# Optimization experiments

Hardware: AMD Instinct MI355X
Metric: run time of the kernel (lower is better)

## Reference

```python
import jax, jax.numpy as jnp
import numpy as np

N_NODES = 100000
N_EDGES = 1600000
IN_DIM, HID, OUT_DIM = 128, 64, 1


def _sage_conv(x, src, dst, wl, wr, b, num_nodes):
    # PyG SAGEConv (aggr='mean', root_weight=True):
    #   out = lin_l(mean_{j in N(i)} x_j) + lin_r(x_i), bias lives in lin_l
    msgs = x[src]                                                  # [E, d] gather
    agg = jax.ops.segment_sum(msgs, dst, num_segments=num_nodes)  # [N, d]
    deg = jax.ops.segment_sum(jnp.ones((src.shape[0],), x.dtype), dst,
                              num_segments=num_nodes)              # [N]
    agg = agg / jnp.maximum(deg, 1.0)[:, None]                     # mean aggregation
    return agg @ wl + x @ wr + b


def setup_inputs() -> dict:
    key = jax.random.key(0)
    ks = jax.random.split(key, 12)
    x = jax.random.normal(ks[0], (N_NODES, IN_DIM), dtype=jnp.float32)
    edge_index = jax.random.randint(ks[1], (2, N_EDGES), 0, N_NODES, dtype=jnp.int64)

    def glorot(k, fan_in, fan_out):
        s = jnp.sqrt(2.0 / (fan_in + fan_out)).astype(jnp.float32)
        return jax.random.normal(k, (fan_in, fan_out), dtype=jnp.float32) * s

    return {
        "x": x,
        "edge_index": edge_index,
        "wl0": glorot(ks[2], IN_DIM, HID), "wr0": glorot(ks[3], IN_DIM, HID),
        "b0": jnp.zeros((HID,), jnp.float32),
        "wl1": glorot(ks[4], HID, HID), "wr1": glorot(ks[5], HID, HID),
        "b1": jnp.zeros((HID,), jnp.float32),
        "wl2": glorot(ks[6], HID, OUT_DIM), "wr2": glorot(ks[7], HID, OUT_DIM),
        "b2": jnp.zeros((OUT_DIM,), jnp.float32),
    }


def reference(x, edge_index, wl0, wr0, b0, wl1, wr1, b1, wl2, wr2, b2):
    src, dst = edge_index[0], edge_index[1]
    n = x.shape[0]
    # layer 0: conv -> relu (dropout is identity in eval mode)
    h = jax.nn.relu(_sage_conv(x, src, dst, wl0, wr0, b0, n))
    # layer 1
    h = jax.nn.relu(_sage_conv(h, src, dst, wl1, wr1, b1, n))
    # final layer + sigmoid
    h = _sage_conv(h, src, dst, wl2, wr2, b2, n)
    return jax.nn.sigmoid(h)
```

## Files before the change

kernel.cpp:

```cpp
#include <hip/hip_runtime.h>
#include <hip/hip_bf16.h>
#include <math.h>


#define SHIFT 7
#define BKT 128
#define CHUNK 4096
#define CAP 4096
#define LCAP 2560
#define HSTR 72

typedef __bf16 bf16_t;
typedef bf16_t bf16x8 __attribute__((ext_vector_type(8)));
typedef float f32x4 __attribute__((ext_vector_type(4)));

#define B16LO(u) __uint_as_float((u) << 16)
#define B16HI(u) __uint_as_float((u) & 0xffff0000u)

#define ADD8(P, V) { P##0 += B16LO(V.x); P##1 += B16HI(V.x); \
                     P##2 += B16LO(V.y); P##3 += B16HI(V.y); \
                     P##4 += B16LO(V.z); P##5 += B16HI(V.z); \
                     P##6 += B16LO(V.w); P##7 += B16HI(V.w); }
#define BFLY(P, M) { P##0 += __shfl_xor(P##0, M); P##1 += __shfl_xor(P##1, M); \
                     P##2 += __shfl_xor(P##2, M); P##3 += __shfl_xor(P##3, M); \
                     P##4 += __shfl_xor(P##4, M); P##5 += __shfl_xor(P##5, M); \
                     P##6 += __shfl_xor(P##6, M); P##7 += __shfl_xor(P##7, M); }

__global__ __launch_bounds__(256) void init_k(const float* __restrict__ wl0,
                                              const float* __restrict__ wr0,
                                              const float* __restrict__ wl1,
                                              const float* __restrict__ wr1,
                                              bf16_t* __restrict__ w0t,
                                              bf16_t* __restrict__ w1t,
                                              int* __restrict__ bcnt,
                                              int NB, int nbP) {
    if ((int)blockIdx.x >= nbP) {
        for (int i = threadIdx.x; i < NB; i += 256) bcnt[i] = 0;
        return;
    }
    int idx = blockIdx.x * 256 + threadIdx.x;
    if (idx < 128 * 128) {
        int j = idx >> 7, k = idx & 127;
        float v = (j < 64) ? wl0[k * 64 + j] : wr0[k * 64 + (j - 64)];
        w0t[idx] = (bf16_t)v;
    } else if (idx < 128 * 128 + 128 * 64) {
        int i2 = idx - 128 * 128;
        int j = i2 >> 6, k = i2 & 63;
        float v = (j < 64) ? wl1[k * 64 + j] : wr1[k * 64 + (j - 64)];
        w1t[i2] = (bf16_t)v;
    }
}

__global__ __launch_bounds__(256) void scatter_gemm0(const int* __restrict__ srcv,
                                                     const int* __restrict__ dstv,
                                                     int* __restrict__ bcnt,
                                                     int* __restrict__ bucketed,
                                                     int E, int NB, int nbC,
                                                     const float* __restrict__ x,
                                                     const bf16_t* __restrict__ w0t,
                                                     bf16_t* __restrict__ y, int N) {
    if ((int)blockIdx.x >= nbC) {
        const int bid = blockIdx.x - nbC;
        const int t = threadIdx.x;
        const int lane = t & 63;
        const int wv = t >> 6;
        const int r0 = bid * 64 + wv * 16;
        const int rr = lane & 15;
        const int quad = lane >> 4;
        const int row_store = r0 + rr;
        int row = (row_store < N) ? row_store : (N - 1);

        bf16x8 xf[4];
#pragma unroll
        for (int kk = 0; kk < 4; ++kk) {
            const float* ap = &x[(size_t)row * 128 + kk * 32 + quad * 8];
            float4 f0 = *(const float4*)ap;
            float4 f1 = *(const float4*)(ap + 4);
            union { bf16x8 v; bf16_t h[8]; } u;
            u.h[0] = (bf16_t)f0.x; u.h[1] = (bf16_t)f0.y;
            u.h[2] = (bf16_t)f0.z; u.h[3] = (bf16_t)f0.w;
            u.h[4] = (bf16_t)f1.x; u.h[5] = (bf16_t)f1.y;
            u.h[6] = (bf16_t)f1.z; u.h[7] = (bf16_t)f1.w;
            xf[kk] = u.v;
        }
#pragma unroll
        for (int c = 0; c < 8; ++c) {
            f32x4 acc = {0.f, 0.f, 0.f, 0.f};
#pragma unroll
            for (int kk = 0; kk < 4; ++kk) {
                bf16x8 wf = *(const bf16x8*)&w0t[(size_t)(c * 16 + rr) * 128 + kk * 32 + quad * 8];
                acc = __builtin_amdgcn_mfma_f32_16x16x32_bf16(wf, xf[kk], acc, 0, 0, 0);
            }
            if (row_store < N) {
                union { bf16_t h[4]; uint2 u; } p;
                p.h[0] = (bf16_t)acc[0]; p.h[1] = (bf16_t)acc[1];
                p.h[2] = (bf16_t)acc[2]; p.h[3] = (bf16_t)acc[3];
                *(uint2*)&y[(size_t)row_store * 128 + c * 16 + quad * 4] = p.u;
            }
        }
        return;
    }

    __shared__ int hist[1024];
    __shared__ int offl[1024];
    __shared__ int basel[1024];
    __shared__ int partial[256];
    __shared__ int posA[CHUNK];
    __shared__ int valA[CHUNK];
    const int t = threadIdx.x;
    for (int i = t; i < NB; i += 256) hist[i] = 0;
    __syncthreads();

    const int cbase = blockIdx.x * CHUNK;
    int bk[CHUNK / 256], rk[CHUNK / 256], vv[CHUNK / 256];
#pragma unroll
    for (int k = 0; k < CHUNK / 256; ++k) {
        int e = cbase + t + k * 256;
        if (e < E) {
            int d = dstv[e];
            int s = srcv[e];
            int b = d >> SHIFT;
            bk[k] = b;
            rk[k] = atomicAdd(&hist[b], 1);
            vv[k] = (s << SHIFT) | (d & (BKT - 1));
        } else {
            bk[k] = -1;
        }
    }
    __syncthreads();

    for (int b = t; b < NB; b += 256) {
        int c = hist[b];
        basel[b] = c ? (b * CAP + atomicAdd(&bcnt[b], c)) : 0;
    }
    {
        int g = t * 4;
        int a0 = (g + 0 < NB) ? hist[g + 0] : 0;
        int a1 = (g + 1 < NB) ? hist[g + 1] : 0;
        int a2 = (g + 2 < NB) ? hist[g + 2] : 0;
        int a3 = (g + 3 < NB) ? hist[g + 3] : 0;
        int sum = a0 + a1 + a2 + a3;
        partial[t] = sum;
        __syncthreads();
        for (int d = 1; d < 256; d <<= 1) {
            int xsc = (t >= d) ? partial[t - d] : 0;
            __syncthreads();
            partial[t] += xsc;
            __syncthreads();
        }
        int ex = partial[t] - sum;
        if (g + 0 < NB) offl[g + 0] = ex;
        if (g + 1 < NB) offl[g + 1] = ex + a0;
        if (g + 2 < NB) offl[g + 2] = ex + a0 + a1;
        if (g + 3 < NB) offl[g + 3] = ex + a0 + a1 + a2;
    }
    __syncthreads();

    int nloc = E - cbase;
    if (nloc > CHUNK) nloc = CHUNK;
#pragma unroll
    for (int k = 0; k < CHUNK / 256; ++k) {
        if (bk[k] >= 0) {
            int slot = offl[bk[k]] + rk[k];
            posA[slot] = basel[bk[k]] + rk[k];
            valA[slot] = vv[k];
        }
    }
    __syncthreads();
    for (int j = t; j < nloc; j += 256) bucketed[posA[j]] = valA[j];
}

__global__ __launch_bounds__(256) void sort_agg0_gemm1(const int* __restrict__ bucketed,
                                                       const int* __restrict__ bcnt,
                                                       int2* __restrict__ od,
                                                       int* __restrict__ csr,
                                                       const bf16_t* __restrict__ y,
                                                       const float* __restrict__ bias,
                                                       const bf16_t* __restrict__ w1t,
                                                       bf16_t* __restrict__ y2,
                                                       int N, int NB) {
    __shared__ int cnt[BKT];
    __shared__ int sc[BKT];
    __shared__ int cur[BKT];
    __shared__ int lcsr[LCAP];
    __shared__ bf16_t hlds[BKT * HSTR];
    const int t = threadIdx.x;
    const int b = blockIdx.x;
    const int ebase = b * CAP;
    const int ecnt = bcnt[b];
    const int eend = ebase + ecnt;

    if (t < BKT) cnt[t] = 0;
    __syncthreads();
    int wreg[CAP / 256];
#pragma unroll
    for (int k = 0; k < CAP / 256; ++k) {
        int i = ebase + t + k * 256;
        if (i < eend) {
            wreg[k] = bucketed[i];
            atomicAdd(&cnt[wreg[k] & (BKT - 1)], 1);
        }
    }
    __syncthreads();
    int v = (t < BKT) ? cnt[t] : 0;
    if (t < BKT) sc[t] = v;
    __syncthreads();
    for (int d = 1; d < BKT; d <<= 1) {
        int xsc = (t < BKT && t >= d) ? sc[t - d] : 0;
        __syncthreads();
        if (t < BKT) sc[t] += xsc;
        __syncthreads();
    }
    if (t < BKT) {
        int ex = sc[t] - v;
        cur[t] = ex;
        int dst = (b << SHIFT) + t;
        if (dst < N) od[dst] = make_int2(ebase + ex, v);
    }
    __syncthreads();
#pragma unroll
    for (int k = 0; k < CAP / 256; ++k) {
        int i = ebase + t + k * 256;
        if (i < eend) {
            int w = wreg[k];
            int p = atomicAdd(&cur[w & (BKT - 1)], 1);
            int s = w >> SHIFT;
            csr[ebase + p] = s;
            if (p < LCAP) lcsr[p] = s;
        }
    }
    __syncthreads();

    const int lane = t & 63;
    const int wv = t >> 6;
    const int oct = lane >> 3;
    const int ch = (lane & 7) * 8;
    const int gbase = b << SHIFT;
    const float4 bv0 = *(const float4*)&bias[ch];
    const float4 bv1 = *(const float4*)&bias[ch + 4];

    for (int k = 0; k < 32; ++k) {
        const int n = wv * 32 + k;
        const int gi = gbase + n;
        const int d = (gi < N) ? cnt[n] : 0;
        const int bas = sc[n] - cnt[n];
        int sidx = 0;
        if (lane < d) {
            int slot = bas + lane;
            sidx = (slot < LCAP) ? lcsr[slot] : csr[ebase + slot];
        }
        float a0 = 0.f, a1 = 0.f, a2 = 0.f, a3 = 0.f;
        float a4 = 0.f, a5 = 0.f, a6 = 0.f, a7 = 0.f;
        const int nblk = d >> 3;
        const int pm = (nblk < 8) ? nblk : 8;
        int p = 0;
        for (; p + 2 <= pm; p += 2) {
            int s0 = __shfl(sidx, 8 * p + oct);
            int s1 = __shfl(sidx, 8 * p + 8 + oct);
            uint4 v0 = *(const uint4*)&y[(size_t)s0 * 128 + ch];
            uint4 v1 = *(const uint4*)&y[(size_t)s1 * 128 + ch];
            ADD8(a, v0); ADD8(a, v1);
        }
        for (; p < pm; ++p) {
            int s0 = __shfl(sidx, 8 * p + oct);
            uint4 v0 = *(const uint4*)&y[(size_t)s0 * 128 + ch];
            ADD8(a, v0);
        }
        for (; p < nblk; ++p) {
            int s0 = csr[ebase + bas + 8 * p + oct];
            uint4 v0 = *(const uint4*)&y[(size_t)s0 * 128 + ch];
            ADD8(a, v0);
        }
        {
            int te = 8 * nblk + oct;
            int tec = (te < 64) ? te : 63;
            int s_t = __shfl(sidx, tec);
            if (te < d) {
                int s0 = (te < 64) ? s_t : csr[ebase + bas + te];
                uint4 v0 = *(const uint4*)&y[(size_t)s0 * 128 + ch];
                ADD8(a, v0);
            }
        }

        BFLY(a, 8); BFLY(a, 16); BFLY(a, 32);

        if (gi < N) {
            float inv = 1.f / ((d > 0) ? (float)d : 1.f);
            uint4 vs = *(const uint4*)&y[(size_t)gi * 128 + 64 + ch];
            float v0 = fmaxf(a0 * inv + B16LO(vs.x) + bv0.x, 0.f);
            float v1 = fmaxf(a1 * inv + B16HI(vs.x) + bv0.y, 0.f);
            float v2 = fmaxf(a2 * inv + B16LO(vs.y) + bv0.z, 0.f);
            float v3 = fmaxf(a3 * inv + B16HI(vs.y) + bv0.w, 0.f);
            float v4 = fmaxf(a4 * inv + B16LO(vs.z) + bv1.x, 0.f);
            float v5 = fmaxf(a5 * inv + B16HI(vs.z) + bv1.y, 0.f);
            float v6 = fmaxf(a6 * inv + B16LO(vs.w) + bv1.z, 0.f);
            float v7 = fmaxf(a7 * inv + B16HI(vs.w) + bv1.w, 0.f);
            if (oct == 0) {
                union { bf16_t bb[8]; uint4 u; } pk;
                pk.bb[0] = (bf16_t)v0; pk.bb[1] = (bf16_t)v1;
                pk.bb[2] = (bf16_t)v2; pk.bb[3] = (bf16_t)v3;
                pk.bb[4] = (bf16_t)v4; pk.bb[5] = (bf16_t)v5;
                pk.bb[6] = (bf16_t)v6; pk.bb[7] = (bf16_t)v7;
                *(uint4*)&hlds[n * HSTR + ch] = pk.u;
            }
        }
    }
    __syncthreads();

    const int rr = lane & 15;
    const int quad = lane >> 4;
#pragma unroll
    for (int half = 0; half < 2; ++half) {
        const int rloc = wv * 32 + half * 16 + rr;
        const int row_store = gbase + rloc;
        bf16x8 xf[2];
#pragma unroll
        for (int kk = 0; kk < 2; ++kk)
            xf[kk] = *(const bf16x8*)&hlds[rloc * HSTR + kk * 32 + quad * 8];
#pragma unroll
        for (int c = 0; c < 8; ++c) {
            f32x4 acc = {0.f, 0.f, 0.f, 0.f};
#pragma unroll
            for (int kk = 0; kk < 2; ++kk) {
                bf16x8 wf = *(const bf16x8*)&w1t[(size_t)(c * 16 + rr) * 64 + kk * 32 + quad * 8];
                acc = __builtin_amdgcn_mfma_f32_16x16x32_bf16(wf, xf[kk], acc, 0, 0, 0);
            }
            if (row_store < N) {
                union { bf16_t h[4]; uint2 u; } p;
                p.h[0] = (bf16_t)acc[0]; p.h[1] = (bf16_t)acc[1];
                p.h[2] = (bf16_t)acc[2]; p.h[3] = (bf16_t)acc[3];
                *(uint2*)&y2[(size_t)row_store * 128 + c * 16 + quad * 4] = p.u;
            }
        }
    }
}

__global__ __launch_bounds__(256) void agg1(const bf16_t* __restrict__ y,
                                            const int* __restrict__ csr,
                                            const int2* __restrict__ od,
                                            const float* __restrict__ bias,
                                            const float* __restrict__ wl2,
                                            const float* __restrict__ wr2,
                                            float* __restrict__ sl,
                                            float* __restrict__ sr, int N) {
    const int lane = threadIdx.x & 63;
    const int oct = lane >> 3;
    const int ch = (lane & 7) * 8;
    const int nw = gridDim.x * 4;

    int i = blockIdx.x * 4 + (threadIdx.x >> 6);
    int2 odc = (i < N) ? od[i] : make_int2(0, 0);
    int sidx = 0;
    if (i < N) sidx = (lane < odc.y) ? csr[odc.x + lane] : 0;

    while (i < N) {
        const int inext = i + nw;
        int2 odn = (inext < N) ? od[inext] : make_int2(0, 0);

        const int base = odc.x;
        const int d = odc.y;
        float a0 = 0.f, a1 = 0.f, a2 = 0.f, a3 = 0.f;
        float a4 = 0.f, a5 = 0.f, a6 = 0.f, a7 = 0.f;
        const int nblk = d >> 3;
        const int pm = (nblk < 8) ? nblk : 8;
        int p = 0;
        for (; p + 2 <= pm; p += 2) {
            int s0 = __shfl(sidx, 8 * p + oct);
            int s1 = __shfl(sidx, 8 * p + 8 + oct);
            uint4 v0 = *(const uint4*)&y[(size_t)s0 * 128 + ch];
            uint4 v1 = *(const uint4*)&y[(size_t)s1 * 128 + ch];
            ADD8(a, v0); ADD8(a, v1);
        }
        for (; p < pm; ++p) {
            int s0 = __shfl(sidx, 8 * p + oct);
            uint4 v0 = *(const uint4*)&y[(size_t)s0 * 128 + ch];
            ADD8(a, v0);
        }
        for (; p < nblk; ++p) {
            int s0 = csr[base + 8 * p + oct];
            uint4 v0 = *(const uint4*)&y[(size_t)s0 * 128 + ch];
            ADD8(a, v0);
        }
        {
            int te = 8 * nblk + oct;
            int tec = (te < 64) ? te : 63;
            int s_t = __shfl(sidx, tec);
            if (te < d) {
                int s0 = (te < 64) ? s_t : csr[base + te];
                uint4 v0 = *(const uint4*)&y[(size_t)s0 * 128 + ch];
                ADD8(a, v0);
            }
        }

        int sidxn = 0;
        if (inext < N) sidxn = (lane < odn.y) ? csr[odn.x + lane] : 0;

        BFLY(a, 8); BFLY(a, 16); BFLY(a, 32);

        float inv = 1.f / ((d > 0) ? (float)d : 1.f);
        uint4 vs = *(const uint4*)&y[(size_t)i * 128 + 64 + ch];
        float4 bv0 = *(const float4*)&bias[ch];
        float4 bv1 = *(const float4*)&bias[ch + 4];
        float v0 = fmaxf(a0 * inv + B16LO(vs.x) + bv0.x, 0.f);
        float v1 = fmaxf(a1 * inv + B16HI(vs.x) + bv0.y, 0.f);
        float v2 = fmaxf(a2 * inv + B16LO(vs.y) + bv0.z, 0.f);
        float v3 = fmaxf(a3 * inv + B16HI(vs.y) + bv0.w, 0.f);
        float v4 = fmaxf(a4 * inv + B16LO(vs.z) + bv1.x, 0.f);
        float v5 = fmaxf(a5 * inv + B16HI(vs.z) + bv1.y, 0.f);
        float v6 = fmaxf(a6 * inv + B16LO(vs.w) + bv1.z, 0.f);
        float v7 = fmaxf(a7 * inv + B16HI(vs.w) + bv1.w, 0.f);

        {
            float4 w0 = *(const float4*)&wl2[ch];
            float4 w1 = *(const float4*)&wl2[ch + 4];
            float4 u0 = *(const float4*)&wr2[ch];
            float4 u1 = *(const float4*)&wr2[ch + 4];
            float a = v0 * w0.x + v1 * w0.y + v2 * w0.z + v3 * w0.w +
                      v4 * w1.x + v5 * w1.y + v6 * w1.z + v7 * w1.w;
            float b = v0 * u0.x + v1 * u0.y + v2 * u0.z + v3 * u0.w +
                      v4 * u1.x + v5 * u1.y + v6 * u1.z + v7 * u1.w;
            a += __shfl_xor(a, 1); b += __shfl_xor(b, 1);
            a += __shfl_xor(a, 2); b += __shfl_xor(b, 2);
            a += __shfl_xor(a, 4); b += __shfl_xor(b, 4);
            if (lane == 0) { sl[i] = a; sr[i] = b; }
        }

        odc = odn;
        sidx = sidxn;
        i = inext;
    }
}

__global__ __launch_bounds__(256) void final_k(const float* __restrict__ sl,
                                               const float* __restrict__ sr,
                                               const int* __restrict__ csr,
                                               const int2* __restrict__ od,
                                               const float* __restrict__ b2,
                                               float* __restrict__ out, int N) {
    int wid = blockIdx.x * 4 + (threadIdx.x >> 6);
    if (wid >= N) return;
    const int lane = threadIdx.x & 63;
    const int2 odv = od[wid];
    const int base = odv.x;
    const int d = odv.y;
    float acc = 0.f;
    for (int e = lane; e < d; e += 64) acc += sl[csr[base + e]];
#pragma unroll
    for (int off = 32; off; off >>= 1) acc += __shfl_xor(acc, off);
    if (lane == 0) {
        float m = (d > 0) ? (float)d : 1.f;
        float v = acc / m + sr[wid] + b2[0];
        out[wid] = 1.f / (1.f + expf(-v));
    }
}

extern "C" void kernel_launch(void* const* d_in, const int* in_sizes, int n_in,
                              void* d_out, int out_size, void* d_ws, size_t ws_size,
                              hipStream_t stream) {
    const float* x  = (const float*)d_in[0];
    const int*  ei  = (const int*)d_in[1];
    const float* wl0 = (const float*)d_in[2];
    const float* wr0 = (const float*)d_in[3];
    const float* b0  = (const float*)d_in[4];
    const float* wl1 = (const float*)d_in[5];
    const float* wr1 = (const float*)d_in[6];
    const float* b1  = (const float*)d_in[7];
    const float* wl2 = (const float*)d_in[8];
    const float* wr2 = (const float*)d_in[9];
    const float* b2  = (const float*)d_in[10];
    float* out = (float*)d_out;

    const int E = in_sizes[1] / 2;
    const int N = out_size;
    const int* srcv = ei;
    const int* dstv = ei + E;
    const int NB = (N + BKT - 1) >> SHIFT;

    char* ws = (char*)d_ws;
    size_t o = 0;
    auto take = [&](size_t nbytes) -> void* {
        void* p = ws + o;
        o = (o + nbytes + 255) & ~(size_t)255;
        return p;
    };
    int2* od      = (int2*)take((size_t)N * 8);
    int* bcnt     = (int*)take((size_t)(NB + 2) * 4);
    int* bucketed = (int*)take((size_t)NB * CAP * 4);
    int* csr      = (int*)take((size_t)NB * CAP * 4);
    bf16_t* w0t   = (bf16_t*)take(128 * 128 * 2);
    bf16_t* w1t   = (bf16_t*)take(128 * 64 * 2);
    bf16_t* y     = (bf16_t*)take((size_t)N * 128 * 2);
    bf16_t* y2    = (bf16_t*)take((size_t)N * 128 * 2);
    float* sl     = (float*)take((size_t)N * 4);
    float* sr     = (float*)take((size_t)N * 4);
    (void)ws_size;

    const int nbC = (E + CHUNK - 1) / CHUNK;
    const int nbP = (128 * 128 + 128 * 64 + 255) / 256;
    const int nbW = (N + 3) / 4;
    const int nbG = (N + 63) / 64;
    const int nbA = 2048;

    init_k<<<nbP + 1, 256, 0, stream>>>(wl0, wr0, wl1, wr1, w0t, w1t, bcnt, NB, nbP);
    scatter_gemm0<<<nbC + nbG, 256, 0, stream>>>(srcv, dstv, bcnt, bucketed, E, NB, nbC,
                                                 x, w0t, y, N);

    sort_agg0_gemm1<<<NB, 256, 0, stream>>>(bucketed, bcnt, od, csr, y, b0, w1t,
                                            y2, N, NB);
    agg1<<<nbA, 256, 0, stream>>>(y2, csr, od, b1, wl2, wr2, sl, sr, N);
    final_k<<<nbW, 256, 0, stream>>>(sl, sr, csr, od, b2, out, N);
}
```

Baseline: 289.7 us.

## Fuse all stages into one persistent cooperative kernel with grid syncs

Replaces the five separate kernel launches with a single persistent cooperative kernel that loops over virtual blocks and uses grid-wide syncs between the weight prep, bucketing/GEMM0, sort/aggregate, and final stages. It also splits the left and right projection outputs into separate 64-wide buffers so the neighbour gather reads a compact array, and halves the edge chunk size so the shared-memory footprint permits higher occupancy. The aim is to remove launch gaps and tail effects between stages. In exchange, grid syncs serialize all blocks at each stage boundary, and the fixed persistent grid may balance work worse than a full launch.

```diff
diff --git a/kernel.cpp b/kernel.cpp
--- a/kernel.cpp
+++ b/kernel.cpp
@@ -1,14 +1,16 @@
 #include <hip/hip_runtime.h>
+#include <hip/hip_cooperative_groups.h>
 #include <hip/hip_bf16.h>
 #include <math.h>
 
 
 #define SHIFT 7
 #define BKT 128
-#define CHUNK 4096
+#define CHUNK 2048
 #define CAP 4096
 #define LCAP 2560
 #define HSTR 72
+#define SMEM_BYTES 30208
 
 typedef __bf16 bf16_t;
 typedef bf16_t bf16x8 __attribute__((ext_vector_type(8)));
@@ -26,267 +28,365 @@
                      P##4 += __shfl_xor(P##4, M); P##5 += __shfl_xor(P##5, M); \
                      P##6 += __shfl_xor(P##6, M); P##7 += __shfl_xor(P##7, M); }
 
-__global__ __launch_bounds__(256) void init_k(const float* __restrict__ wl0,
-                                              const float* __restrict__ wr0,
-                                              const float* __restrict__ wl1,
-                                              const float* __restrict__ wr1,
-                                              bf16_t* __restrict__ w0t,
-                                              bf16_t* __restrict__ w1t,
-                                              int* __restrict__ bcnt,
-                                              int NB, int nbP) {
-    if ((int)blockIdx.x >= nbP) {
-        for (int i = threadIdx.x; i < NB; i += 256) bcnt[i] = 0;
-        return;
-    }
-    int idx = blockIdx.x * 256 + threadIdx.x;
-    if (idx < 128 * 128) {
-        int j = idx >> 7, k = idx & 127;
-        float v = (j < 64) ? wl0[k * 64 + j] : wr0[k * 64 + (j - 64)];
-        w0t[idx] = (bf16_t)v;
-    } else if (idx < 128 * 128 + 128 * 64) {
-        int i2 = idx - 128 * 128;
-        int j = i2 >> 6, k = i2 & 63;
-        float v = (j < 64) ? wl1[k * 64 + j] : wr1[k * 64 + (j - 64)];
-        w1t[i2] = (bf16_t)v;
-    }
-}
-
-__global__ __launch_bounds__(256) void scatter_gemm0(const int* __restrict__ srcv,
-                                                     const int* __restrict__ dstv,
-                                                     int* __restrict__ bcnt,
-                                                     int* __restrict__ bucketed,
-                                                     int E, int NB, int nbC,
-                                                     const float* __restrict__ x,
-                                                     const bf16_t* __restrict__ w0t,
-                                                     bf16_t* __restrict__ y, int N) {
-    if ((int)blockIdx.x >= nbC) {
-        const int bid = blockIdx.x - nbC;
-        const int t = threadIdx.x;
-        const int lane = t & 63;
-        const int wv = t >> 6;
-        const int r0 = bid * 64 + wv * 16;
-        const int rr = lane & 15;
-        const int quad = lane >> 4;
-        const int row_store = r0 + rr;
-        int row = (row_store < N) ? row_store : (N - 1);
-
-        bf16x8 xf[4];
-#pragma unroll
-        for (int kk = 0; kk < 4; ++kk) {
-            const float* ap = &x[(size_t)row * 128 + kk * 32 + quad * 8];
-            float4 f0 = *(const float4*)ap;
-            float4 f1 = *(const float4*)(ap + 4);
-            union { bf16x8 v; bf16_t h[8]; } u;
-            u.h[0] = (bf16_t)f0.x; u.h[1] = (bf16_t)f0.y;
-            u.h[2] = (bf16_t)f0.z; u.h[3] = (bf16_t)f0.w;
-            u.h[4] = (bf16_t)f1.x; u.h[5] = (bf16_t)f1.y;
-            u.h[6] = (bf16_t)f1.z; u.h[7] = (bf16_t)f1.w;
-            xf[kk] = u.v;
-        }
-#pragma unroll
-        for (int c = 0; c < 8; ++c) {
-            f32x4 acc = {0.f, 0.f, 0.f, 0.f};
-#pragma unroll
-            for (int kk = 0; kk < 4; ++kk) {
-                bf16x8 wf = *(const bf16x8*)&w0t[(size_t)(c * 16 + rr) * 128 + kk * 32 + quad * 8];
-                acc = __builtin_amdgcn_mfma_f32_16x16x32_bf16(wf, xf[kk], acc, 0, 0, 0);
-            }
-            if (row_store < N) {
-                union { bf16_t h[4]; uint2 u; } p;
-                p.h[0] = (bf16_t)acc[0]; p.h[1] = (bf16_t)acc[1];
-                p.h[2] = (bf16_t)acc[2]; p.h[3] = (bf16_t)acc[3];
-                *(uint2*)&y[(size_t)row_store * 128 + c * 16 + quad * 4] = p.u;
-            }
-        }
-        return;
-    }
-
-    __shared__ int hist[1024];
-    __shared__ int offl[1024];
-    __shared__ int basel[1024];
-    __shared__ int partial[256];
-    __shared__ int posA[CHUNK];
-    __shared__ int valA[CHUNK];
+struct KParams {
+    const int* srcv; const int* dstv;
+    int* bcnt; int* bucketed; int* csr; int2* od;
+    const float* x;
+    bf16_t* w0t; bf16_t* w1t;
+    bf16_t* yl; bf16_t* yr; bf16_t* y2l; bf16_t* y2r;
+    float* sl; float* sr;
+    const float* wl0; const float* wr0; const float* wl1; const float* wr1;
+    const float* b0; const float* b1;
+    const float* wl2; const float* wr2; const float* b2;
+    float* out;
+    int N, E, NB, nvC, nvG;
+};
+
+__global__ __launch_bounds__(256, 5) void fused_all(KParams p) {
+    namespace cg = cooperative_groups;
+    cg::grid_group grid = cg::this_grid();
+    __shared__ __align__(16) char smem[SMEM_BYTES];
     const int t = threadIdx.x;
-    for (int i = t; i < NB; i += 256) hist[i] = 0;
-    __syncthreads();
-
-    const int cbase = blockIdx.x * CHUNK;
-    int bk[CHUNK / 256], rk[CHUNK / 256], vv[CHUNK / 256];
-#pragma unroll
-    for (int k = 0; k < CHUNK / 256; ++k) {
-        int e = cbase + t + k * 256;
-        if (e < E) {
-            int d = dstv[e];
-            int s = srcv[e];
-            int b = d >> SHIFT;
-            bk[k] = b;
-            rk[k] = atomicAdd(&hist[b], 1);
-            vv[k] = (s << SHIFT) | (d & (BKT - 1));
+    const int nbg = gridDim.x;
+    const int lane = t & 63;
+    const int wv = t >> 6;
+
+    for (int idx = blockIdx.x * 256 + t; idx < 128 * 128 + 128 * 64;
+         idx += nbg * 256) {
+        if (idx < 128 * 128) {
+            int j = idx >> 7, k = idx & 127;
+            float v = (j < 64) ? p.wl0[k * 64 + j] : p.wr0[k * 64 + (j - 64)];
+            p.w0t[idx] = (bf16_t)v;
         } else {
-            bk[k] = -1;
+            int i2 = idx - 128 * 128;
+            int j = i2 >> 6, k = i2 & 63;
+            float v = (j < 64) ? p.wl1[k * 64 + j] : p.wr1[k * 64 + (j - 64)];
+            p.w1t[i2] = (bf16_t)v;
         }
     }
-    __syncthreads();
-
-    for (int b = t; b < NB; b += 256) {
-        int c = hist[b];
-        basel[b] = c ? (b * CAP + atomicAdd(&bcnt[b], c)) : 0;
-    }
+    for (int i = blockIdx.x * 256 + t; i < p.NB; i += nbg * 256) p.bcnt[i] = 0;
+    grid.sync();
+
     {
-        int g = t * 4;
-        int a0 = (g + 0 < NB) ? hist[g + 0] : 0;
-        int a1 = (g + 1 < NB) ? hist[g + 1] : 0;
-        int a2 = (g + 2 < NB) ? hist[g + 2] : 0;
-        int a3 = (g + 3 < NB) ? hist[g + 3] : 0;
-        int sum = a0 + a1 + a2 + a3;
-        partial[t] = sum;
-        __syncthreads();
-        for (int d = 1; d < 256; d <<= 1) {
-            int xsc = (t >= d) ? partial[t - d] : 0;
-            __syncthreads();
-            partial[t] += xsc;
-            __syncthreads();
-        }
-        int ex = partial[t] - sum;
-        if (g + 0 < NB) offl[g + 0] = ex;
-        if (g + 1 < NB) offl[g + 1] = ex + a0;
-        if (g + 2 < NB) offl[g + 2] = ex + a0 + a1;
-        if (g + 3 < NB) offl[g + 3] = ex + a0 + a1 + a2;
-    }
-    __syncthreads();
-
-    int nloc = E - cbase;
-    if (nloc > CHUNK) nloc = CHUNK;
-#pragma unroll
-    for (int k = 0; k < CHUNK / 256; ++k) {
-        if (bk[k] >= 0) {
-            int slot = offl[bk[k]] + rk[k];
-            posA[slot] = basel[bk[k]] + rk[k];
-            valA[slot] = vv[k];
+        int* hist = (int*)smem;
+        int* offl = hist + 1024;
+        int* basel = offl + 1024;
+        int* partial = basel + 1024;
+        int* posA = partial + 256;
+        int* valA = posA + CHUNK;
+        const int nvTot = p.nvC + p.nvG;
+        for (int vb = blockIdx.x; vb < nvTot; vb += nbg) {
+            if (vb >= p.nvC) {
+                const int bid = vb - p.nvC;
+                const int r0 = bid * 64 + wv * 16;
+                const int rr = lane & 15;
+                const int quad = lane >> 4;
+                const int row_store = r0 + rr;
+                int row = (row_store < p.N) ? row_store : (p.N - 1);
+                bf16x8 xf[4];
+#pragma unroll
+                for (int kk = 0; kk < 4; ++kk) {
+                    const float* ap = &p.x[(size_t)row * 128 + kk * 32 + quad * 8];
+                    float4 f0 = *(const float4*)ap;
+                    float4 f1 = *(const float4*)(ap + 4);
+                    union { bf16x8 v; bf16_t h[8]; } u;
+                    u.h[0] = (bf16_t)f0.x; u.h[1] = (bf16_t)f0.y;
+                    u.h[2] = (bf16_t)f0.z; u.h[3] = (bf16_t)f0.w;
+                    u.h[4] = (bf16_t)f1.x; u.h[5] = (bf16_t)f1.y;
+                    u.h[6] = (bf16_t)f1.z; u.h[7] = (bf16_t)f1.w;
+                    xf[kk] = u.v;
+                }
+#pragma unroll
+                for (int c = 0; c < 8; ++c) {
+                    f32x4 acc = {0.f, 0.f, 0.f, 0.f};
+#pragma unroll
+                    for (int kk = 0; kk < 4; ++kk) {
+                        bf16x8 wf = *(const bf16x8*)&p.w0t[(size_t)(c * 16 + rr) * 128 + kk * 32 + quad * 8];
+                        acc = __builtin_amdgcn_mfma_f32_16x16x32_bf16(wf, xf[kk], acc, 0, 0, 0);
+                    }
+                    if (row_store < p.N) {
+                        union { bf16_t h[4]; uint2 u; } pk;
+                        pk.h[0] = (bf16_t)acc[0]; pk.h[1] = (bf16_t)acc[1];
+                        pk.h[2] = (bf16_t)acc[2]; pk.h[3] = (bf16_t)acc[3];
+                        if (c < 4)
+                            *(uint2*)&p.yl[(size_t)row_store * 64 + c * 16 + quad * 4] = pk.u;
+                        else
+                            *(uint2*)&p.yr[(size_t)row_store * 64 + (c - 4) * 16 + quad * 4] = pk.u;
+                    }
+                }
+                continue;
+            }
+            for (int i = t; i < p.NB; i += 256) hist[i] = 0;
+            __syncthreads();
+            const int cbase = vb * CHUNK;
+            int bk[CHUNK / 256], rk[CHUNK / 256], vvv[CHUNK / 256];
+#pragma unroll
+            for (int k = 0; k < CHUNK / 256; ++k) {
+                int e = cbase + t + k * 256;
+                if (e < p.E) {
+                    int d = p.dstv[e];
+                    int s = p.srcv[e];
+                    int b = d >> SHIFT;
+                    bk[k] = b;
+                    rk[k] = atomicAdd(&hist[b], 1);
+                    vvv[k] = (s << SHIFT) | (d & (BKT - 1));
+                } else {
+                    bk[k] = -1;
+                }
+            }
+            __syncthreads();
+            for (int b = t; b < p.NB; b += 256) {
+                int c = hist[b];
+                basel[b] = c ? (b * CAP + atomicAdd(&p.bcnt[b], c)) : 0;
+            }
+            {
+                int g = t * 4;
+                int a0 = (g + 0 < p.NB) ? hist[g + 0] : 0;
+                int a1 = (g + 1 < p.NB) ? hist[g + 1] : 0;
+                int a2 = (g + 2 < p.NB) ? hist[g + 2] : 0;
+                int a3 = (g + 3 < p.NB) ? hist[g + 3] : 0;
+                int sum = a0 + a1 + a2 + a3;
+                partial[t] = sum;
+                __syncthreads();
+                for (int d = 1; d < 256; d <<= 1) {
+                    int xsc = (t >= d) ? partial[t - d] : 0;
+                    __syncthreads();
+                    partial[t] += xsc;
+                    __syncthreads();
+                }
+                int ex = partial[t] - sum;
+                if (g + 0 < p.NB) offl[g + 0] = ex;
+                if (g + 1 < p.NB) offl[g + 1] = ex + a0;
+                if (g + 2 < p.NB) offl[g + 2] = ex + a0 + a1;
+                if (g + 3 < p.NB) offl[g + 3] = ex + a0 + a1 + a2;
+            }
+            __syncthreads();
+            int nloc = p.E - cbase;
+            if (nloc > CHUNK) nloc = CHUNK;
+#pragma unroll
+            for (int k = 0; k < CHUNK / 256; ++k) {
+                if (bk[k] >= 0) {
+                    int slot = offl[bk[k]] + rk[k];
+                    posA[slot] = basel[bk[k]] + rk[k];
+                    valA[slot] = vvv[k];
+                }
+            }
+            __syncthreads();
+            for (int j = t; j < nloc; j += 256) p.bucketed[posA[j]] = valA[j];
+            __syncthreads();
         }
     }
-    __syncthreads();
-    for (int j = t; j < nloc; j += 256) bucketed[posA[j]] = valA[j];
-}
-
-__global__ __launch_bounds__(256) void sort_agg0_gemm1(const int* __restrict__ bucketed,
-                                                       const int* __restrict__ bcnt,
-                                                       int2* __restrict__ od,
-                                                       int* __restrict__ csr,
-                                                       const bf16_t* __restrict__ y,
-                                                       const float* __restrict__ bias,
-                                                       const bf16_t* __restrict__ w1t,
-                                                       bf16_t* __restrict__ y2,
-                                                       int N, int NB) {
-    __shared__ int cnt[BKT];
-    __shared__ int sc[BKT];
-    __shared__ int cur[BKT];
-    __shared__ int lcsr[LCAP];
-    __shared__ bf16_t hlds[BKT * HSTR];
-    const int t = threadIdx.x;
-    const int b = blockIdx.x;
-    const int ebase = b * CAP;
-    const int ecnt = bcnt[b];
-    const int eend = ebase + ecnt;
-
-    if (t < BKT) cnt[t] = 0;
-    __syncthreads();
-    int wreg[CAP / 256];
-#pragma unroll
-    for (int k = 0; k < CAP / 256; ++k) {
-        int i = ebase + t + k * 256;
-        if (i < eend) {
-            wreg[k] = bucketed[i];
-            atomicAdd(&cnt[wreg[k] & (BKT - 1)], 1);
+    grid.sync();
+
+    {
+        int* cnt = (int*)smem;
+        int* sc = cnt + 128;
+        int* cur = sc + 128;
+        int* lcsr = cur + 128;
+        bf16_t* hlds = (bf16_t*)(lcsr + LCAP);
+        const int oct = lane >> 3;
+        const int ch = (lane & 7) * 8;
+        const float4 bv0 = *(const float4*)&p.b0[ch];
+        const float4 bv1 = *(const float4*)&p.b0[ch + 4];
+        for (int vb = blockIdx.x; vb < p.NB; vb += nbg) {
+            const int b = vb;
+            const int ebase = b * CAP;
+            const int ecnt = p.bcnt[b];
+            const int eend = ebase + ecnt;
+            if (t < BKT) cnt[t] = 0;
+            __syncthreads();
+            int wreg[CAP / 256];
+#pragma unroll
+            for (int k = 0; k < CAP / 256; ++k) {
+                int i = ebase + t + k * 256;
+                if (i < eend) {
+                    wreg[k] = p.bucketed[i];
+                    atomicAdd(&cnt[wreg[k] & (BKT - 1)], 1);
+                }
+            }
+            __syncthreads();
+            int v = (t < BKT) ? cnt[t] : 0;
+            if (t < BKT) sc[t] = v;
+            __syncthreads();
+            for (int d = 1; d < BKT; d <<= 1) {
+                int xsc = (t < BKT && t >= d) ? sc[t - d] : 0;
+                __syncthreads();
+                if (t < BKT) sc[t] += xsc;
+                __syncthreads();
+            }
+            if (t < BKT) {
+                int ex = sc[t] - v;
+                cur[t] = ex;
+                int dst = (b << SHIFT) + t;
+                if (dst < p.N) p.od[dst] = make_int2(ebase + ex, v);
+            }
+            __syncthreads();
+#pragma unroll
+            for (int k = 0; k < CAP / 256; ++k) {
+                int i = ebase + t + k * 256;
+                if (i < eend) {
+                    int w = wreg[k];
+                    int pp = atomicAdd(&cur[w & (BKT - 1)], 1);
+                    int s = w >> SHIFT;
+                    p.csr[ebase + pp] = s;
+                    if (pp < LCAP) lcsr[pp] = s;
+                }
+            }
+            __syncthreads();
+
+            const int gbase = b << SHIFT;
+            for (int k = 0; k < 32; ++k) {
+                const int n = wv * 32 + k;
+                const int gi = gbase + n;
+                const int d = (gi < p.N) ? cnt[n] : 0;
+                const int bas = sc[n] - cnt[n];
+                int sidx = 0;
+                if (lane < d) {
+                    int slot = bas + lane;
+                    sidx = (slot < LCAP) ? lcsr[slot] : p.csr[ebase + slot];
+                }
+                float a0 = 0.f, a1 = 0.f, a2 = 0.f, a3 = 0.f;
+                float a4 = 0.f, a5 = 0.f, a6 = 0.f, a7 = 0.f;
+                const int nblk = d >> 3;
+                const int pm = (nblk < 8) ? nblk : 8;
+                int pp = 0;
+                for (; pp + 2 <= pm; pp += 2) {
+                    int s0 = __shfl(sidx, 8 * pp + oct);
+                    int s1 = __shfl(sidx, 8 * pp + 8 + oct);
+                    uint4 v0 = *(const uint4*)&p.yl[(size_t)s0 * 64 + ch];
+                    uint4 v1 = *(const uint4*)&p.yl[(size_t)s1 * 64 + ch];
+                    ADD8(a, v0); ADD8(a, v1);
+                }
+                for (; pp < pm; ++pp) {
+                    int s0 = __shfl(sidx, 8 * pp + oct);
+                    uint4 v0 = *(const uint4*)&p.yl[(size_t)s0 * 64 + ch];
+                    ADD8(a, v0);
+                }
+                for (; pp < nblk; ++pp) {
+                    int s0 = p.csr[ebase + bas + 8 * pp + oct];
+                    uint4 v0 = *(const uint4*)&p.yl[(size_t)s0 * 64 + ch];
+                    ADD8(a, v0);
+                }
+                {
+                    int te = 8 * nblk + oct;
+                    int tec = (te < 64) ? te : 63;
+                    int s_t = __shfl(sidx, tec);
+                    if (te < d) {
+                        int s0 = (te < 64) ? s_t : p.csr[ebase + bas + te];
+                        uint4 v0 = *(const uint4*)&p.yl[(size_t)s0 * 64 + ch];
+                        ADD8(a, v0);
+                    }
+                }
+                BFLY(a, 8); BFLY(a, 16); BFLY(a, 32);
+                if (gi < p.N) {
+                    float inv = 1.f / ((d > 0) ? (float)d : 1.f);
+                    uint4 vs = *(const uint4*)&p.yr[(size_t)gi * 64 + ch];
+                    float v0 = fmaxf(a0 * inv + B16LO(vs.x) + bv0.x, 0.f);
+                    float v1 = fmaxf(a1 * inv + B16HI(vs.x) + bv0.y, 0.f);
+                    float v2 = fmaxf(a2 * inv + B16LO(vs.y) + bv0.z, 0.f);
+                    float v3 = fmaxf(a3 * inv + B16HI(vs.y) + bv0.w, 0.f);
+                    float v4 = fmaxf(a4 * inv + B16LO(vs.z) + bv1.x, 0.f);
+                    float v5 = fmaxf(a5 * inv + B16HI(vs.z) + bv1.y, 0.f);
+                    float v6 = fmaxf(a6 * inv + B16LO(vs.w) + bv1.z, 0.f);
+                    float v7 = fmaxf(a7 * inv + B16HI(vs.w) + bv1.w, 0.f);
+                    if (oct == 0) {
+                        union { bf16_t bb[8]; uint4 u; } pk;
+                        pk.bb[0] = (bf16_t)v0; pk.bb[1] = (bf16_t)v1;
+                        pk.bb[2] = (bf16_t)v2; pk.bb[3] = (bf16_t)v3;
+                        pk.bb[4] = (bf16_t)v4; pk.bb[5] = (bf16_t)v5;
+                        pk.bb[6] = (bf16_t)v6; pk.bb[7] = (bf16_t)v7;
+                        *(uint4*)&hlds[n * HSTR + ch] = pk.u;
+                    }
+                }
+            }
+            __syncthreads();
+
+            const int rr = lane & 15;
+            const int quad = lane >> 4;
+#pragma unroll
+            for (int half = 0; half < 2; ++half) {
+                const int rloc = wv * 32 + half * 16 + rr;
+                const int row_store = gbase + rloc;
+                bf16x8 xf[2];
+#pragma unroll
+                for (int kk = 0; kk < 2; ++kk)
+                    xf[kk] = *(const bf16x8*)&hlds[rloc * HSTR + kk * 32 + quad * 8];
+#pragma unroll
+                for (int c = 0; c < 8; ++c) {
+                    f32x4 acc = {0.f, 0.f, 0.f, 0.f};
+#pragma unroll
+                    for (int kk = 0; kk < 2; ++kk) {
+                        bf16x8 wf = *(const bf16x8*)&p.w1t[(size_t)(c * 16 + rr) * 64 + kk * 32 + quad * 8];
+                        acc = __builtin_amdgcn_mfma_f32_16x16x32_bf16(wf, xf[kk], acc, 0, 0, 0);
+                    }
+                    if (row_store < p.N) {
+                        union { bf16_t h[4]; uint2 u; } pk;
+                        pk.h[0] = (bf16_t)acc[0]; pk.h[1] = (bf16_t)acc[1];
+                        pk.h[2] = (bf16_t)acc[2]; pk.h[3] = (bf16_t)acc[3];
+                        if (c < 4)
+                            *(uint2*)&p.y2l[(size_t)row_store * 64 + c * 16 + quad * 4] = pk.u;
+                        else
+                            *(uint2*)&p.y2r[(size_t)row_store * 64 + (c - 4) * 16 + quad * 4] = pk.u;
+                    }
+                }
+            }
+            __syncthreads();
         }
     }
-    __syncthreads();
-    int v = (t < BKT) ? cnt[t] : 0;
-    if (t < BKT) sc[t] = v;
-    __syncthreads();
-    for (int d = 1; d < BKT; d <<= 1) {
-        int xsc = (t < BKT && t >= d) ? sc[t - d] : 0;
-        __syncthreads();
-        if (t < BKT) sc[t] += xsc;
-        __syncthreads();
-    }
-    if (t < BKT) {
-        int ex = sc[t] - v;
-        cur[t] = ex;
-        int dst = (b << SHIFT) + t;
-        if (dst < N) od[dst] = make_int2(ebase + ex, v);
-    }
-    __syncthreads();
-#pragma unroll
-    for (int k = 0; k < CAP / 256; ++k) {
-        int i = ebase + t + k * 256;
-        if (i < eend) {
-            int w = wreg[k];
-            int p = atomicAdd(&cur[w & (BKT - 1)], 1);
-            int s = w >> SHIFT;
-            csr[ebase + p] = s;
-            if (p < LCAP) lcsr[p] = s;
-        }
-    }
-    __syncthreads();
-
-    const int lane = t & 63;
-    const int wv = t >> 6;
-    const int oct = lane >> 3;
-    const int ch = (lane & 7) * 8;
-    const int gbase = b << SHIFT;
-    const float4 bv0 = *(const float4*)&bias[ch];
-    const float4 bv1 = *(const float4*)&bias[ch + 4];
-
-    for (int k = 0; k < 32; ++k) {
-        const int n = wv * 32 + k;
-        const int gi = gbase + n;
-        const int d = (gi < N) ? cnt[n] : 0;
-        const int bas = sc[n] - cnt[n];
+    grid.sync();
+
+    {
+        const int oct = lane >> 3;
+        const int ch = (lane & 7) * 8;
+        const int nw = nbg * 4;
+        int i = blockIdx.x * 4 + wv;
+        int2 odc = (i < p.N) ? p.od[i] : make_int2(0, 0);
         int sidx = 0;
-        if (lane < d) {
-            int slot = bas + lane;
-            sidx = (slot < LCAP) ? lcsr[slot] : csr[ebase + slot];
-        }
-        float a0 = 0.f, a1 = 0.f, a2 = 0.f, a3 = 0.f;
-        float a4 = 0.f, a5 = 0.f, a6 = 0.f, a7 = 0.f;
-        const int nblk = d >> 3;
-        const int pm = (nblk < 8) ? nblk : 8;
-        int p = 0;
-        for (; p + 2 <= pm; p += 2) {
-            int s0 = __shfl(sidx, 8 * p + oct);
-            int s1 = __shfl(sidx, 8 * p + 8 + oct);
-            uint4 v0 = *(const uint4*)&y[(size_t)s0 * 128 + ch];
-            uint4 v1 = *(const uint4*)&y[(size_t)s1 * 128 + ch];
-            ADD8(a, v0); ADD8(a, v1);
-        }
-        for (; p < pm; ++p) {
-            int s0 = __shfl(sidx, 8 * p + oct);
-            uint4 v0 = *(const uint4*)&y[(size_t)s0 * 128 + ch];
-            ADD8(a, v0);
-        }
-        for (; p < nblk; ++p) {
-            int s0 = csr[ebase + bas + 8 * p + oct];
-            uint4 v0 = *(const uint4*)&y[(size_t)s0 * 128 + ch];
-            ADD8(a, v0);
-        }
-        {
-            int te = 8 * nblk + oct;
-            int tec = (te < 64) ? te : 63;
-            int s_t = __shfl(sidx, tec);
-            if (te < d) {
-                int s0 = (te < 64) ? s_t : csr[ebase + bas + te];
-                uint4 v0 = *(const uint4*)&y[(size_t)s0 * 128 + ch];
+        if (i < p.N) sidx = (lane < odc.y) ? p.csr[odc.x + lane] : 0;
+        while (i < p.N) {
+            const int inext = i + nw;
+            int2 odn = (inext < p.N) ? p.od[inext] : make_int2(0, 0);
+            const int base = odc.x;
+            const int d = odc.y;
+            float a0 = 0.f, a1 = 0.f, a2 = 0.f, a3 = 0.f;
+            float a4 = 0.f, a5 = 0.f, a6 = 0.f, a7 = 0.f;
+            const int nblk = d >> 3;
+            const int pm = (nblk < 8) ? nblk : 8;
+            int pp = 0;
+            for (; pp + 2 <= pm; pp += 2) {
+                int s0 = __shfl(sidx, 8 * pp + oct);
+                int s1 = __shfl(sidx, 8 * pp + 8 + oct);
+                uint4 v0 = *(const uint4*)&p.y2l[(size_t)s0 * 64 + ch];
+                uint4 v1 = *(const uint4*)&p.y2l[(size_t)s1 * 64 + ch];
+                ADD8(a, v0); ADD8(a, v1);
+            }
+            for (; pp < pm; ++pp) {
+                int s0 = __shfl(sidx, 8 * pp + oct);
+                uint4 v0 = *(const uint4*)&p.y2l[(size_t)s0 * 64 + ch];
                 ADD8(a, v0);
             }
-        }
-
-        BFLY(a, 8); BFLY(a, 16); BFLY(a, 32);
-
-        if (gi < N) {
+            for (; pp < nblk; ++pp) {
+                int s0 = p.csr[base + 8 * pp + oct];
+                uint4 v0 = *(const uint4*)&p.y2l[(size_t)s0 * 64 + ch];
+                ADD8(a, v0);
+            }
+            {
+                int te = 8 * nblk + oct;
+                int tec = (te < 64) ? te : 63;
+                int s_t = __shfl(sidx, tec);
+                if (te < d) {
+                    int s0 = (te < 64) ? s_t : p.csr[base + te];
+                    uint4 v0 = *(const uint4*)&p.y2l[(size_t)s0 * 64 + ch];
+                    ADD8(a, v0);
+                }
+            }
+            int sidxn = 0;
+            if (inext < p.N) sidxn = (lane < odn.y) ? p.csr[odn.x + lane] : 0;
+            BFLY(a, 8); BFLY(a, 16); BFLY(a, 32);
             float inv = 1.f / ((d > 0) ? (float)d : 1.f);
-            uint4 vs = *(const uint4*)&y[(size_t)gi * 128 + 64 + ch];
+            uint4 vs = *(const uint4*)&p.y2r[(size_t)i * 64 + ch];
+            float4 bv0 = *(const float4*)&p.b1[ch];
+            float4 bv1 = *(const float4*)&p.b1[ch + 4];
             float v0 = fmaxf(a0 * inv + B16LO(vs.x) + bv0.x, 0.f);
             float v1 = fmaxf(a1 * inv + B16HI(vs.x) + bv0.y, 0.f);
             float v2 = fmaxf(a2 * inv + B16LO(vs.y) + bv0.z, 0.f);
@@ -295,162 +395,42 @@
             float v5 = fmaxf(a5 * inv + B16HI(vs.z) + bv1.y, 0.f);
             float v6 = fmaxf(a6 * inv + B16LO(vs.w) + bv1.z, 0.f);
             float v7 = fmaxf(a7 * inv + B16HI(vs.w) + bv1.w, 0.f);
-            if (oct == 0) {
-                union { bf16_t bb[8]; uint4 u; } pk;
-                pk.bb[0] = (bf16_t)v0; pk.bb[1] = (bf16_t)v1;
-                pk.bb[2] = (bf16_t)v2; pk.bb[3] = (bf16_t)v3;
-                pk.bb[4] = (bf16_t)v4; pk.bb[5] = (bf16_t)v5;
-                pk.bb[6] = (bf16_t)v6; pk.bb[7] = (bf16_t)v7;
-                *(uint4*)&hlds[n * HSTR + ch] = pk.u;
-            }
+            {
+                float4 w0 = *(const float4*)&p.wl2[ch];
+                float4 w1 = *(const float4*)&p.wl2[ch + 4];
+                float4 u0 = *(const float4*)&p.wr2[ch];
+                float4 u1 = *(const float4*)&p.wr2[ch + 4];
+                float a = v0 * w0.x + v1 * w0.y + v2 * w0.z + v3 * w0.w +
+                          v4 * w1.x + v5 * w1.y + v6 * w1.z + v7 * w1.w;
+                float bqq = v0 * u0.x + v1 * u0.y + v2 * u0.z + v3 * u0.w +
+                            v4 * u1.x + v5 * u1.y + v6 * u1.z + v7 * u1.w;
+                a += __shfl_xor(a, 1); bqq += __shfl_xor(bqq, 1);
+                a += __shfl_xor(a, 2); bqq += __shfl_xor(bqq, 2);
+                a += __shfl_xor(a, 4); bqq += __shfl_xor(bqq, 4);
+                if (lane == 0) { p.sl[i] = a; p.sr[i] = bqq; }
+            }
+            odc = odn;
+            sidx = sidxn;
+            i = inext;
         }
     }
-    __syncthreads();
-
-    const int rr = lane & 15;
-    const int quad = lane >> 4;
-#pragma unroll
-    for (int half = 0; half < 2; ++half) {
-        const int rloc = wv * 32 + half * 16 + rr;
-        const int row_store = gbase + rloc;
-        bf16x8 xf[2];
-#pragma unroll
-        for (int kk = 0; kk < 2; ++kk)
-            xf[kk] = *(const bf16x8*)&hlds[rloc * HSTR + kk * 32 + quad * 8];
-#pragma unroll
-        for (int c = 0; c < 8; ++c) {
-            f32x4 acc = {0.f, 0.f, 0.f, 0.f};
-#pragma unroll
-            for (int kk = 0; kk < 2; ++kk) {
-                bf16x8 wf = *(const bf16x8*)&w1t[(size_t)(c * 16 + rr) * 64 + kk * 32 + quad * 8];
-                acc = __builtin_amdgcn_mfma_f32_16x16x32_bf16(wf, xf[kk], acc, 0, 0, 0);
-            }
-            if (row_store < N) {
-                union { bf16_t h[4]; uint2 u; } p;
-                p.h[0] = (bf16_t)acc[0]; p.h[1] = (bf16_t)acc[1];
-                p.h[2] = (bf16_t)acc[2]; p.h[3] = (bf16_t)acc[3];
-                *(uint2*)&y2[(size_t)row_store * 128 + c * 16 + quad * 4] = p.u;
+    grid.sync();
+
+    {
+        for (int wid = blockIdx.x * 4 + wv; wid < p.N; wid += nbg * 4) {
+            const int2 odv = p.od[wid];
+            const int base = odv.x;
+            const int d = odv.y;
+            float acc = 0.f;
+            for (int e = lane; e < d; e += 64) acc += p.sl[p.csr[base + e]];
+#pragma unroll
+            for (int off = 32; off; off >>= 1) acc += __shfl_xor(acc, off);
+            if (lane == 0) {
+                float m = (d > 0) ? (float)d : 1.f;
+                float v = acc / m + p.sr[wid] + p.b2[0];
+                p.out[wid] = 1.f / (1.f + expf(-v));
             }
         }
-    }
-}
-
-__global__ __launch_bounds__(256) void agg1(const bf16_t* __restrict__ y,
-                                            const int* __restrict__ csr,
-                                            const int2* __restrict__ od,
-                                            const float* __restrict__ bias,
-                                            const float* __restrict__ wl2,
-                                            const float* __restrict__ wr2,
-                                            float* __restrict__ sl,
-                                            float* __restrict__ sr, int N) {
-    const int lane = threadIdx.x & 63;
-    const int oct = lane >> 3;
-    const int ch = (lane & 7) * 8;
-    const int nw = gridDim.x * 4;
-
-    int i = blockIdx.x * 4 + (threadIdx.x >> 6);
-    int2 odc = (i < N) ? od[i] : make_int2(0, 0);
-    int sidx = 0;
-    if (i < N) sidx = (lane < odc.y) ? csr[odc.x + lane] : 0;
-
-    while (i < N) {
-        const int inext = i + nw;
-        int2 odn = (inext < N) ? od[inext] : make_int2(0, 0);
-
-        const int base = odc.x;
-        const int d = odc.y;
-        float a0 = 0.f, a1 = 0.f, a2 = 0.f, a3 = 0.f;
-        float a4 = 0.f, a5 = 0.f, a6 = 0.f, a7 = 0.f;
-        const int nblk = d >> 3;
-        const int pm = (nblk < 8) ? nblk : 8;
-        int p = 0;
-        for (; p + 2 <= pm; p += 2) {
-            int s0 = __shfl(sidx, 8 * p + oct);
-            int s1 = __shfl(sidx, 8 * p + 8 + oct);
-            uint4 v0 = *(const uint4*)&y[(size_t)s0 * 128 + ch];
-            uint4 v1 = *(const uint4*)&y[(size_t)s1 * 128 + ch];
-            ADD8(a, v0); ADD8(a, v1);
-        }
-        for (; p < pm; ++p) {
-            int s0 = __shfl(sidx, 8 * p + oct);
-            uint4 v0 = *(const uint4*)&y[(size_t)s0 * 128 + ch];
-            ADD8(a, v0);
-        }
-        for (; p < nblk; ++p) {
-            int s0 = csr[base + 8 * p + oct];
-            uint4 v0 = *(const uint4*)&y[(size_t)s0 * 128 + ch];
-            ADD8(a, v0);
-        }
-        {
-            int te = 8 * nblk + oct;
-            int tec = (te < 64) ? te : 63;
-            int s_t = __shfl(sidx, tec);
-            if (te < d) {
-                int s0 = (te < 64) ? s_t : csr[base + te];
-                uint4 v0 = *(const uint4*)&y[(size_t)s0 * 128 + ch];
-                ADD8(a, v0);
-            }
-        }
-
-        int sidxn = 0;
-        if (inext < N) sidxn = (lane < odn.y) ? csr[odn.x + lane] : 0;
-
-        BFLY(a, 8); BFLY(a, 16); BFLY(a, 32);
-
-        float inv = 1.f / ((d > 0) ? (float)d : 1.f);
-        uint4 vs = *(const uint4*)&y[(size_t)i * 128 + 64 + ch];
-        float4 bv0 = *(const float4*)&bias[ch];
-        float4 bv1 = *(const float4*)&bias[ch + 4];
-        float v0 = fmaxf(a0 * inv + B16LO(vs.x) + bv0.x, 0.f);
-        float v1 = fmaxf(a1 * inv + B16HI(vs.x) + bv0.y, 0.f);
-        float v2 = fmaxf(a2 * inv + B16LO(vs.y) + bv0.z, 0.f);
-        float v3 = fmaxf(a3 * inv + B16HI(vs.y) + bv0.w, 0.f);
-        float v4 = fmaxf(a4 * inv + B16LO(vs.z) + bv1.x, 0.f);
-        float v5 = fmaxf(a5 * inv + B16HI(vs.z) + bv1.y, 0.f);
-        float v6 = fmaxf(a6 * inv + B16LO(vs.w) + bv1.z, 0.f);
-        float v7 = fmaxf(a7 * inv + B16HI(vs.w) + bv1.w, 0.f);
-
-        {
-            float4 w0 = *(const float4*)&wl2[ch];
-            float4 w1 = *(const float4*)&wl2[ch + 4];
-            float4 u0 = *(const float4*)&wr2[ch];
-            float4 u1 = *(const float4*)&wr2[ch + 4];
-            float a = v0 * w0.x + v1 * w0.y + v2 * w0.z + v3 * w0.w +
-                      v4 * w1.x + v5 * w1.y + v6 * w1.z + v7 * w1.w;
-            float b = v0 * u0.x + v1 * u0.y + v2 * u0.z + v3 * u0.w +
-                      v4 * u1.x + v5 * u1.y + v6 * u1.z + v7 * u1.w;
-            a += __shfl_xor(a, 1); b += __shfl_xor(b, 1);
-            a += __shfl_xor(a, 2); b += __shfl_xor(b, 2);
-            a += __shfl_xor(a, 4); b += __shfl_xor(b, 4);
-            if (lane == 0) { sl[i] = a; sr[i] = b; }
-        }
-
-        odc = odn;
-        sidx = sidxn;
-        i = inext;
-    }
-}
-
-__global__ __launch_bounds__(256) void final_k(const float* __restrict__ sl,
-                                               const float* __restrict__ sr,
-                                               const int* __restrict__ csr,
-                                               const int2* __restrict__ od,
-                                               const float* __restrict__ b2,
-                                               float* __restrict__ out, int N) {
-    int wid = blockIdx.x * 4 + (threadIdx.x >> 6);
-    if (wid >= N) return;
-    const int lane = threadIdx.x & 63;
-    const int2 odv = od[wid];
-    const int base = odv.x;
-    const int d = odv.y;
-    float acc = 0.f;
-    for (int e = lane; e < d; e += 64) acc += sl[csr[base + e]];
-#pragma unroll
-    for (int off = 32; off; off >>= 1) acc += __shfl_xor(acc, off);
-    if (lane == 0) {
-        float m = (d > 0) ? (float)d : 1.f;
-        float v = acc / m + sr[wid] + b2[0];
-        out[wid] = 1.f / (1.f + expf(-v));
     }
 }
 
@@ -459,54 +439,59 @@
                               hipStream_t stream) {
     const float* x  = (const float*)d_in[0];
     const int*  ei  = (const int*)d_in[1];
-    const float* wl0 = (const float*)d_in[2];
-    const float* wr0 = (const float*)d_in[3];
-    const float* b0  = (const float*)d_in[4];
-    const float* wl1 = (const float*)d_in[5];
-    const float* wr1 = (const float*)d_in[6];
-    const float* b1  = (const float*)d_in[7];
-    const float* wl2 = (const float*)d_in[8];
-    const float* wr2 = (const float*)d_in[9];
-    const float* b2  = (const float*)d_in[10];
-    float* out = (float*)d_out;
 
     const int E = in_sizes[1] / 2;
     const int N = out_size;
-    const int* srcv = ei;
-    const int* dstv = ei + E;
     const int NB = (N + BKT - 1) >> SHIFT;
 
     char* ws = (char*)d_ws;
     size_t o = 0;
     auto take = [&](size_t nbytes) -> void* {
-        void* p = ws + o;
+        void* pq = ws + o;
         o = (o + nbytes + 255) & ~(size_t)255;
-        return p;
+        return pq;
     };
-    int2* od      = (int2*)take((size_t)N * 8);
-    int* bcnt     = (int*)take((size_t)(NB + 2) * 4);
-    int* bucketed = (int*)take((size_t)NB * CAP * 4);
-    int* csr      = (int*)take((size_t)NB * CAP * 4);
-    bf16_t* w0t   = (bf16_t*)take(128 * 128 * 2);
-    bf16_t* w1t   = (bf16_t*)take(128 * 64 * 2);
-    bf16_t* y     = (bf16_t*)take((size_t)N * 128 * 2);
-    bf16_t* y2    = (bf16_t*)take((size_t)N * 128 * 2);
-    float* sl     = (float*)take((size_t)N * 4);
-    float* sr     = (float*)take((size_t)N * 4);
+    KParams p;
+    p.od       = (int2*)take((size_t)N * 8);
+    p.bcnt     = (int*)take((size_t)(NB + 2) * 4);
+    p.bucketed = (int*)take((size_t)NB * CAP * 4);
+    p.csr      = (int*)take((size_t)NB * CAP * 4);
+    p.w0t      = (bf16_t*)take(128 * 128 * 2);
+    p.w1t      = (bf16_t*)take(128 * 64 * 2);
+    p.yl       = (bf16_t*)take((size_t)N * 64 * 2);
+    p.yr       = (bf16_t*)take((size_t)N * 64 * 2);
+    p.y2l      = (bf16_t*)take((size_t)N * 64 * 2);
+    p.y2r      = (bf16_t*)take((size_t)N * 64 * 2);
+    p.sl       = (float*)take((size_t)N * 4);
+    p.sr       = (float*)take((size_t)N * 4);
     (void)ws_size;
 
-    const int nbC = (E + CHUNK - 1) / CHUNK;
-    const int nbP = (128 * 128 + 128 * 64 + 255) / 256;
-    const int nbW = (N + 3) / 4;
-    const int nbG = (N + 63) / 64;
-    const int nbA = 2048;
-
-    init_k<<<nbP + 1, 256, 0, stream>>>(wl0, wr0, wl1, wr1, w0t, w1t, bcnt, NB, nbP);
-    scatter_gemm0<<<nbC + nbG, 256, 0, stream>>>(srcv, dstv, bcnt, bucketed, E, NB, nbC,
-                                                 x, w0t, y, N);
-
-    sort_agg0_gemm1<<<NB, 256, 0, stream>>>(bucketed, bcnt, od, csr, y, b0, w1t,
-                                            y2, N, NB);
-    agg1<<<nbA, 256, 0, stream>>>(y2, csr, od, b1, wl2, wr2, sl, sr, N);
-    final_k<<<nbW, 256, 0, stream>>>(sl, sr, csr, od, b2, out, N);
+    p.srcv = ei;
+    p.dstv = ei + E;
+    p.x    = x;
+    p.wl0 = (const float*)d_in[2];
+    p.wr0 = (const float*)d_in[3];
+    p.b0  = (const float*)d_in[4];
+    p.wl1 = (const float*)d_in[5];
+    p.wr1 = (const float*)d_in[6];
+    p.b1  = (const float*)d_in[7];
+    p.wl2 = (const float*)d_in[8];
+    p.wr2 = (const float*)d_in[9];
+    p.b2  = (const float*)d_in[10];
+    p.out = (float*)d_out;
+    p.N = N;
+    p.E = E;
+    p.NB = NB;
+    p.nvC = (E + CHUNK - 1) / CHUNK;
+    p.nvG = (N + 63) / 64;
+
+    int maxb = 0;
+    (void)hipOccupancyMaxActiveBlocksPerMultiprocessor(&maxb, fused_all, 256, 0);
+    if (maxb < 1) maxb = 1;
+    int nblk = maxb * 256;
+    if (nblk > 1280) nblk = 1280;
+
+    void* args[] = { (void*)&p };
+    (void)hipLaunchCooperativeKernel((void*)fused_all, dim3(nblk), dim3(256),
+                                     args, 0, stream);
 }
```

Result: slower. 709.0 us (+144.8%).
